# Optimization experiments

Hardware: AMD Instinct MI355X
Metric: run time of the kernel (lower is better)

The kernel has to match this reference:

```python
import jax, jax.numpy as jnp
import numpy as np

B, T, C, H = 8, 2048, 1024, 128

def setup_inputs() -> dict:
    key = jax.random.key(0)
    kx, kq, kk, kv = jax.random.split(key, 4)
    x = jax.random.normal(kx, (B, T, C), dtype=jnp.float32)
    Wq = jax.random.normal(kq, (C, H), dtype=jnp.float32) * 0.02
    Wk = jax.random.normal(kk, (C, H), dtype=jnp.float32) * 0.02
    Wv = jax.random.normal(kv, (C, H), dtype=jnp.float32) * 0.02
    return {"x": x, "Wq": Wq, "Wk": Wk, "Wv": Wv}

def reference(x, Wq, Wk, Wv):
    # q,k,v: [B,T,H] via bias-free dense projections
    q = jnp.einsum('btc,ch->bth', x, Wq)
    k = jnp.einsum('btc,ch->bth', x, Wk)
    v = jnp.einsum('btc,ch->bth', x, Wv)
    scale = k.shape[-1] ** (-0.5)
    # scores: [B,T,T]
    wei = jnp.einsum('bth,bsh->bts', q, k) * scale
    Tlen = x.shape[1]
    causal = jnp.tril(jnp.ones((Tlen, Tlen), dtype=bool))  # True = keep
    wei = jnp.where(causal[None, :, :], wei, -jnp.inf)
    wei = jax.nn.softmax(wei, axis=-1)
    return jnp.einsum('bts,bsh->bth', wei, v)
```

## Files before the change

### kernel.cpp

```cpp
#include <hip/hip_runtime.h>

#define B_ 8
#define T_ 2048
#define C_ 1024
#define H_ 128
#define BT_ (B_*T_)

typedef unsigned short u16;
typedef unsigned int u32;
typedef __attribute__((ext_vector_type(4))) float f32x4;
typedef __attribute__((ext_vector_type(8))) __bf16 bf16x8;

__device__ __forceinline__ u16 f2bf(float f) {
  u32 u = __float_as_uint(f);
  u += 0x7fffu + ((u >> 16) & 1u);
  return (u16)(u >> 16);
}

#define GLL16(g, l) __builtin_amdgcn_global_load_lds( \
    (const __attribute__((address_space(1))) void*)(g), \
    (__attribute__((address_space(3))) void*)(l), 16, 0, 0)

__device__ __forceinline__ bf16x8 load_frag(const u16* base, int stride, int row0, int k0, int lane) {
  const u16* p = base + (size_t)(row0 + (lane & 15)) * stride + k0 + ((lane >> 4) << 3);
  return *reinterpret_cast<const bf16x8*>(p);
}

__device__ __forceinline__ bf16x8 cvt8n(f32x4 lo, f32x4 hi) {
  bf16x8 r;
#pragma unroll
  for (int i = 0; i < 4; i++) { r[i] = (__bf16)lo[i]; r[4 + i] = (__bf16)hi[i]; }
  return r;
}

__global__ void wt_kernel(const float* __restrict__ Wq, const float* __restrict__ Wk,
                          const float* __restrict__ Wv, u16* __restrict__ wt) {
  int mat = blockIdx.y;
  const float* W = (mat == 0) ? Wq : (mat == 1) ? Wk : Wv;
  int i = blockIdx.x * 256 + threadIdx.x;
  int h = i >> 10;
  int c = i & 1023;
  wt[mat * (C_ * H_) + i] = f2bf(W[c * H_ + h]);
}

__global__ __launch_bounds__(512, 4) void qkv_gemm(const float* __restrict__ x, const u16* __restrict__ wt,
                                                   u16* __restrict__ q, u16* __restrict__ k2,
                                                   u16* __restrict__ vt) {
  __shared__ __align__(16) float As[2][64 * 64];
  __shared__ __align__(16) u16 Bs[2][192 * 64];
  int t = threadIdx.x;
  int lane = t & 63, w = t >> 6;
  int wm = w >> 2, wn = w & 3;
  int quad = lane >> 4, col = lane & 15;
  int m0 = blockIdx.x * 64;
  int nb = blockIdx.y * 192;

  int arow = t >> 4;
  int acg = (t & 15) ^ (arow & 15);
  const float* ax0 = x + (size_t)(m0 + arow) * C_ + acg * 4;
  const float* ax1 = ax0 + (size_t)32 * C_;
  int brow = t >> 3;
  int bcg = (t & 7) ^ (brow & 7);
  const u16* bw0 = wt + (size_t)(nb + brow) * C_ + bcg * 8;
  const u16* bw1 = bw0 + (size_t)64 * C_;
  const u16* bw2 = bw0 + (size_t)128 * C_;

#define STAGE(st, buf) do { \
    int ko_ = (st) * 64; \
    GLL16(ax0 + ko_, &As[buf][t * 4]); \
    GLL16(ax1 + ko_, &As[buf][2048 + t * 4]); \
    GLL16(bw0 + ko_, &Bs[buf][t * 8]); \
    GLL16(bw1 + ko_, &Bs[buf][4096 + t * 8]); \
    GLL16(bw2 + ko_, &Bs[buf][8192 + t * 8]); \
  } while (0)

  STAGE(0, 0);

  f32x4 acc[2][3] = {};
#pragma unroll 2
  for (int kk = 0; kk < 16; kk++) {
    int cur = kk & 1;
    __syncthreads();
    if (kk + 1 < 16) STAGE(kk + 1, cur ^ 1);
    const float* Ab = &As[cur][0];
    const u16* Bb = &Bs[cur][0];
#pragma unroll
    for (int ks = 0; ks < 2; ks++) {
      bf16x8 af[2], bfr[3];
#pragma unroll
      for (int mt = 0; mt < 2; mt++) {
        int rr = wm * 32 + mt * 16 + col;
        int s0 = (ks * 8 + quad * 2) ^ (rr & 15);
        int s1 = s0 ^ 1;
        f32x4 lo = *reinterpret_cast<const f32x4*>(Ab + rr * 64 + s0 * 4);
        f32x4 hi = *reinterpret_cast<const f32x4*>(Ab + rr * 64 + s1 * 4);
        af[mt] = cvt8n(lo, hi);
      }
#pragma unroll
      for (int nt = 0; nt < 3; nt++) {
        int rr = wn * 48 + nt * 16 + col;
        int sl = (ks * 4 + quad) ^ (rr & 7);
        bfr[nt] = *reinterpret_cast<const bf16x8*>(Bb + rr * 64 + sl * 8);
      }
#pragma unroll
      for (int mt = 0; mt < 2; mt++)
#pragma unroll
        for (int nt = 0; nt < 3; nt++)
          acc[mt][nt] = __builtin_amdgcn_mfma_f32_16x16x32_bf16(af[mt], bfr[nt], acc[mt][nt], 0, 0, 0);
    }
  }
#undef STAGE

#pragma unroll
  for (int mt = 0; mt < 2; mt++) {
    int row0 = m0 + wm * 32 + mt * 16 + quad * 4;
#pragma unroll
    for (int nt = 0; nt < 3; nt++) {
      int n = nb + wn * 48 + nt * 16 + col;
      int mat = n >> 7, h = n & 127;
      if (mat == 0) {
#pragma unroll
        for (int r = 0; r < 4; r++) q[(size_t)(row0 + r) * H_ + h] = f2bf(acc[mt][nt][r]);
      } else if (mat == 1) {
#pragma unroll
        for (int r = 0; r < 4; r++) k2[(size_t)(row0 + r) * H_ + h] = f2bf(acc[mt][nt][r]);
      } else {
        int bb = row0 >> 11, tt = row0 & 2047;
        ushort4 pk;
        pk.x = f2bf(acc[mt][nt][0]); pk.y = f2bf(acc[mt][nt][1]);
        pk.z = f2bf(acc[mt][nt][2]); pk.w = f2bf(acc[mt][nt][3]);
        *reinterpret_cast<ushort4*>(&vt[((size_t)bb * H_ + h) * T_ + tt]) = pk;
      }
    }
  }
}

__global__ __launch_bounds__(512, 4) void attn_part(const u16* __restrict__ q, const u16* __restrict__ k,
                                                    const u16* __restrict__ vt,
                                                    float* __restrict__ Op, float* __restrict__ lsum) {
  __shared__ __align__(16) u16 Ks[2][32 * 132];
  __shared__ __align__(16) u16 Vs[2][128 * 36];
  __shared__ __align__(16) u16 P[8][16 * 40];
  int t = threadIdx.x;
  int lane = t & 63, w = t >> 6;
  int quad = lane >> 4, col = lane & 15;
  int bx = blockIdx.x;
  int qt = 15 - (bx >> 5);
  int s = (bx >> 3) & 3;
  int b = bx & 7;
  const float scale = 0.08838834764831845f;

  int it0 = s * (qt + 1);
  int it1 = it0 + (qt + 1);

  int krow = t >> 4, ke = (t & 15) * 8;
  int vrow = t >> 2, ve = (t & 3) * 8;

  int qrow0 = b * T_ + qt * 128 + w * 16;
  bf16x8 qf[4];
#pragma unroll
  for (int ks = 0; ks < 4; ks++) qf[ks] = load_frag(q, H_, qrow0, ks * 32, lane);

  f32x4 o[8] = {};
  float l[4] = {0.f, 0.f, 0.f, 0.f};
  int myqrow = qt * 128 + w * 16 + quad * 4;

  {
    const u16* kb = k + (size_t)(b * T_ + it0 * 32) * H_;
    *reinterpret_cast<uint4*>(&Ks[0][krow * 132 + ke]) = *reinterpret_cast<const uint4*>(kb + (size_t)krow * 128 + ke);
    const u16* vb = vt + (size_t)b * H_ * T_ + it0 * 32;
    *reinterpret_cast<uint4*>(&Vs[0][vrow * 36 + ve]) = *reinterpret_cast<const uint4*>(vb + (size_t)vrow * T_ + ve);
  }

  for (int kt = it0; kt < it1; kt++) {
    int cur = (kt - it0) & 1;
    __syncthreads();
    bool more = (kt + 1 < it1);
    uint4 kc, vc;
    if (more) {
      const u16* kb = k + (size_t)(b * T_ + (kt + 1) * 32) * H_;
      kc = *reinterpret_cast<const uint4*>(kb + (size_t)krow * 128 + ke);
      const u16* vb = vt + (size_t)b * H_ * T_ + (kt + 1) * 32;
      vc = *reinterpret_cast<const uint4*>(vb + (size_t)vrow * T_ + ve);
    }

    f32x4 s0 = {}, s1 = {};
#pragma unroll
    for (int ks = 0; ks < 4; ks++) {
      bf16x8 kb0 = *reinterpret_cast<const bf16x8*>(&Ks[cur][col * 132 + ks * 32 + quad * 8]);
      bf16x8 kb1 = *reinterpret_cast<const bf16x8*>(&Ks[cur][(col + 16) * 132 + ks * 32 + quad * 8]);
      s0 = __builtin_amdgcn_mfma_f32_16x16x32_bf16(qf[ks], kb0, s0, 0, 0, 0);
      s1 = __builtin_amdgcn_mfma_f32_16x16x32_bf16(qf[ks], kb1, s1, 0, 0, 0);
    }

    float pv[8];
    int kcol0 = kt * 32 + col;
#pragma unroll
    for (int r = 0; r < 4; r++) {
      int qr = myqrow + r;
      float a0 = fminf(s0[r] * scale, 30.f);
      float a1 = fminf(s1[r] * scale, 30.f);
      a0 = (kcol0      > qr) ? -1e30f : a0;
      a1 = (kcol0 + 16 > qr) ? -1e30f : a1;
      float p0 = __expf(a0);
      float p1 = __expf(a1);
      pv[r] = p0; pv[4 + r] = p1;
      l[r] += p0 + p1;
    }

    u16* Pb = &P[w][0];
#pragma unroll
    for (int r = 0; r < 4; r++) {
      Pb[(quad * 4 + r) * 40 + col] = f2bf(pv[r]);
      Pb[(quad * 4 + r) * 40 + col + 16] = f2bf(pv[4 + r]);
    }
    asm volatile("" ::: "memory");
    __builtin_amdgcn_s_waitcnt(0xc07f);
    asm volatile("" ::: "memory");
    bf16x8 pf = *reinterpret_cast<const bf16x8*>(&Pb[col * 40 + (quad << 3)]);

#pragma unroll
    for (int ht = 0; ht < 8; ht++) {
      bf16x8 vf = *reinterpret_cast<const bf16x8*>(&Vs[cur][(ht * 16 + col) * 36 + quad * 8]);
      o[ht] = __builtin_amdgcn_mfma_f32_16x16x32_bf16(pf, vf, o[ht], 0, 0, 0);
    }

    if (more) {
      int nxt = cur ^ 1;
      *reinterpret_cast<uint4*>(&Ks[nxt][krow * 132 + ke]) = kc;
      *reinterpret_cast<uint4*>(&Vs[nxt][vrow * 36 + ve]) = vc;
    }
  }

#pragma unroll
  for (int r = 0; r < 4; r++) {
    float v = l[r];
    v += __shfl_xor(v, 1);
    v += __shfl_xor(v, 2);
    v += __shfl_xor(v, 4);
    v += __shfl_xor(v, 8);
    l[r] = v;
  }

  int tile = (s * 8 + b) * 16 + qt;
  float* Orow = Op + (size_t)tile * (128 * 128);
  float* lrow = lsum + (size_t)tile * 128;
  int rowin0 = w * 16 + quad * 4;
  if (col == 0) {
#pragma unroll
    for (int r = 0; r < 4; r++) lrow[rowin0 + r] = l[r];
  }
#pragma unroll
  for (int ht = 0; ht < 8; ht++) {
#pragma unroll
    for (int r = 0; r < 4; r++)
      Orow[(size_t)(rowin0 + r) * 128 + ht * 16 + col] = o[ht][r];
  }
}

__global__ __launch_bounds__(256) void attn_comb(const float* __restrict__ Op, const float* __restrict__ lsum,
                                                 float* __restrict__ out) {
  int bx = blockIdx.x;
  int b = bx >> 4, qt = bx & 15;
  int t = threadIdx.x;
  int h = t & 127, half = t >> 7;
  int tile0 = b * 16 + qt;
#pragma unroll 4
  for (int rr = 0; rr < 64; rr++) {
    int row = half * 64 + rr;
    float ls = 0.f, v = 0.f;
#pragma unroll
    for (int p = 0; p < 4; p++) {
      int tp = tile0 + p * 128;
      ls += lsum[tp * 128 + row];
      v  += Op[(size_t)tp * 16384 + row * 128 + h];
    }
    out[((size_t)(b * T_ + qt * 128 + row)) * H_ + h] = v / ls;
  }
}

extern "C" void kernel_launch(void* const* d_in, const int* in_sizes, int n_in,
                              void* d_out, int out_size, void* d_ws, size_t ws_size,
                              hipStream_t stream) {
  (void)in_sizes; (void)n_in; (void)out_size; (void)ws_size;
  const float* x  = (const float*)d_in[0];
  const float* Wq = (const float*)d_in[1];
  const float* Wk = (const float*)d_in[2];
  const float* Wv = (const float*)d_in[3];
  u16* ws = (u16*)d_ws;
  u16* q  = ws;
  u16* k  = ws + (size_t)BT_ * H_;
  u16* vt = ws + 2 * (size_t)BT_ * H_;
  u16* wt = ws + 3 * (size_t)BT_ * H_;
  float* Op = (float*)(ws + 3 * (size_t)BT_ * H_ + 3 * C_ * H_);
  float* lsum = Op + (size_t)512 * 128 * 128;
  float* out = (float*)d_out;

  wt_kernel<<<dim3(512, 3), 256, 0, stream>>>(Wq, Wk, Wv, wt);
  qkv_gemm<<<dim3(BT_ / 64, 2), 512, 0, stream>>>(x, wt, q, k, vt);
  attn_part<<<dim3(512), 512, 0, stream>>>(q, k, vt, Op, lsum);
  attn_comb<<<dim3(128), 256, 0, stream>>>(Op, lsum, out);
}
```

Measured before the change: 157.9 us.

## Give each attention wave two query sub-tiles to reuse K/V fragments

The attention kernel now runs 256 threads (4 waves) per block, and each wave handles 32 query rows as two 16-row halves instead of 16. Each K and V fragment read from shared memory now feeds two MFMAs, which halves LDS reads per MFMA and doubles the K/V tile loads per thread. LDS padding changes (row strides 136 and 40), and P is stored as packed bf16 pairs in 32-bit words, with a shuffle/unpack step rebuilding the MFMA operand. This raises register use (two sets of accumulators and Q fragments) and gives fewer waves per block, which may reduce occupancy and latency hiding.

Result: no change. 160.0 us (+1.3%).

```diff
diff --git a/kernel.cpp b/kernel.cpp
--- a/kernel.cpp
+++ b/kernel.cpp
@@ -135,12 +135,12 @@
   }
 }
 
-__global__ __launch_bounds__(512, 4) void attn_part(const u16* __restrict__ q, const u16* __restrict__ k,
+__global__ __launch_bounds__(256, 2) void attn_part(const u16* __restrict__ q, const u16* __restrict__ k,
                                                     const u16* __restrict__ vt,
                                                     float* __restrict__ Op, float* __restrict__ lsum) {
-  __shared__ __align__(16) u16 Ks[2][32 * 132];
-  __shared__ __align__(16) u16 Vs[2][128 * 36];
-  __shared__ __align__(16) u16 P[8][16 * 40];
+  __shared__ __align__(16) u16 Ks[2][32 * 136];
+  __shared__ __align__(16) u16 Vs[2][128 * 40];
+  __shared__ __align__(16) u32 P32[4][2][16 * 20];
   int t = threadIdx.x;
   int lane = t & 63, w = t >> 6;
   int quad = lane >> 4, col = lane & 15;
@@ -153,108 +153,139 @@
   int it0 = s * (qt + 1);
   int it1 = it0 + (qt + 1);
 
-  int krow = t >> 4, ke = (t & 15) * 8;
-  int vrow = t >> 2, ve = (t & 3) * 8;
-
-  int qrow0 = b * T_ + qt * 128 + w * 16;
-  bf16x8 qf[4];
-#pragma unroll
-  for (int ks = 0; ks < 4; ks++) qf[ks] = load_frag(q, H_, qrow0, ks * 32, lane);
-
-  f32x4 o[8] = {};
-  float l[4] = {0.f, 0.f, 0.f, 0.f};
-  int myqrow = qt * 128 + w * 16 + quad * 4;
+  int krow0 = t >> 4, ke = (t & 15) * 8;
+  int krow1 = krow0 + 16;
+  int vrow0 = t >> 2, ve = (t & 3) * 8;
+  int vrow1 = vrow0 + 64;
+
+  int qrow0 = b * T_ + qt * 128 + w * 32;
+  bf16x8 qf[2][4];
+#pragma unroll
+  for (int hf = 0; hf < 2; hf++)
+#pragma unroll
+    for (int ks = 0; ks < 4; ks++)
+      qf[hf][ks] = load_frag(q, H_, qrow0 + hf * 16, ks * 32, lane);
+
+  f32x4 o[2][8] = {};
+  float l[8] = {};
+  int myqrow = qt * 128 + w * 32 + quad * 4;
 
   {
     const u16* kb = k + (size_t)(b * T_ + it0 * 32) * H_;
-    *reinterpret_cast<uint4*>(&Ks[0][krow * 132 + ke]) = *reinterpret_cast<const uint4*>(kb + (size_t)krow * 128 + ke);
+    *reinterpret_cast<uint4*>(&Ks[0][krow0 * 136 + ke]) = *reinterpret_cast<const uint4*>(kb + (size_t)krow0 * 128 + ke);
+    *reinterpret_cast<uint4*>(&Ks[0][krow1 * 136 + ke]) = *reinterpret_cast<const uint4*>(kb + (size_t)krow1 * 128 + ke);
     const u16* vb = vt + (size_t)b * H_ * T_ + it0 * 32;
-    *reinterpret_cast<uint4*>(&Vs[0][vrow * 36 + ve]) = *reinterpret_cast<const uint4*>(vb + (size_t)vrow * T_ + ve);
+    *reinterpret_cast<uint4*>(&Vs[0][vrow0 * 40 + ve]) = *reinterpret_cast<const uint4*>(vb + (size_t)vrow0 * T_ + ve);
+    *reinterpret_cast<uint4*>(&Vs[0][vrow1 * 40 + ve]) = *reinterpret_cast<const uint4*>(vb + (size_t)vrow1 * T_ + ve);
   }
 
   for (int kt = it0; kt < it1; kt++) {
     int cur = (kt - it0) & 1;
     __syncthreads();
     bool more = (kt + 1 < it1);
-    uint4 kc, vc;
+    uint4 kc0, kc1, vc0, vc1;
     if (more) {
       const u16* kb = k + (size_t)(b * T_ + (kt + 1) * 32) * H_;
-      kc = *reinterpret_cast<const uint4*>(kb + (size_t)krow * 128 + ke);
+      kc0 = *reinterpret_cast<const uint4*>(kb + (size_t)krow0 * 128 + ke);
+      kc1 = *reinterpret_cast<const uint4*>(kb + (size_t)krow1 * 128 + ke);
       const u16* vb = vt + (size_t)b * H_ * T_ + (kt + 1) * 32;
-      vc = *reinterpret_cast<const uint4*>(vb + (size_t)vrow * T_ + ve);
-    }
-
-    f32x4 s0 = {}, s1 = {};
+      vc0 = *reinterpret_cast<const uint4*>(vb + (size_t)vrow0 * T_ + ve);
+      vc1 = *reinterpret_cast<const uint4*>(vb + (size_t)vrow1 * T_ + ve);
+    }
+
+    f32x4 s0[2] = {}, s1[2] = {};
 #pragma unroll
     for (int ks = 0; ks < 4; ks++) {
-      bf16x8 kb0 = *reinterpret_cast<const bf16x8*>(&Ks[cur][col * 132 + ks * 32 + quad * 8]);
-      bf16x8 kb1 = *reinterpret_cast<const bf16x8*>(&Ks[cur][(col + 16) * 132 + ks * 32 + quad * 8]);
-      s0 = __builtin_amdgcn_mfma_f32_16x16x32_bf16(qf[ks], kb0, s0, 0, 0, 0);
-      s1 = __builtin_amdgcn_mfma_f32_16x16x32_bf16(qf[ks], kb1, s1, 0, 0, 0);
-    }
-
-    float pv[8];
+      bf16x8 kb0 = *reinterpret_cast<const bf16x8*>(&Ks[cur][col * 136 + ks * 32 + quad * 8]);
+      bf16x8 kb1 = *reinterpret_cast<const bf16x8*>(&Ks[cur][(col + 16) * 136 + ks * 32 + quad * 8]);
+#pragma unroll
+      for (int hf = 0; hf < 2; hf++) {
+        s0[hf] = __builtin_amdgcn_mfma_f32_16x16x32_bf16(qf[hf][ks], kb0, s0[hf], 0, 0, 0);
+        s1[hf] = __builtin_amdgcn_mfma_f32_16x16x32_bf16(qf[hf][ks], kb1, s1[hf], 0, 0, 0);
+      }
+    }
+
     int kcol0 = kt * 32 + col;
 #pragma unroll
-    for (int r = 0; r < 4; r++) {
-      int qr = myqrow + r;
-      float a0 = fminf(s0[r] * scale, 30.f);
-      float a1 = fminf(s1[r] * scale, 30.f);
-      a0 = (kcol0      > qr) ? -1e30f : a0;
-      a1 = (kcol0 + 16 > qr) ? -1e30f : a1;
-      float p0 = __expf(a0);
-      float p1 = __expf(a1);
-      pv[r] = p0; pv[4 + r] = p1;
-      l[r] += p0 + p1;
-    }
-
-    u16* Pb = &P[w][0];
-#pragma unroll
-    for (int r = 0; r < 4; r++) {
-      Pb[(quad * 4 + r) * 40 + col] = f2bf(pv[r]);
-      Pb[(quad * 4 + r) * 40 + col + 16] = f2bf(pv[4 + r]);
+    for (int hf = 0; hf < 2; hf++) {
+      u32* Pb = &P32[w][hf][0];
+#pragma unroll
+      for (int r = 0; r < 4; r++) {
+        int qr = myqrow + hf * 16 + r;
+        float a0 = fminf(s0[hf][r] * scale, 30.f);
+        float a1 = fminf(s1[hf][r] * scale, 30.f);
+        a0 = (kcol0      > qr) ? -1e30f : a0;
+        a1 = (kcol0 + 16 > qr) ? -1e30f : a1;
+        float p0 = __expf(a0);
+        float p1 = __expf(a1);
+        l[hf * 4 + r] += p0 + p1;
+        Pb[(quad * 4 + r) * 20 + col] = (u32)f2bf(p0) | ((u32)f2bf(p1) << 16);
+      }
     }
     asm volatile("" ::: "memory");
     __builtin_amdgcn_s_waitcnt(0xc07f);
     asm volatile("" ::: "memory");
-    bf16x8 pf = *reinterpret_cast<const bf16x8*>(&Pb[col * 40 + (quad << 3)]);
+
+    bf16x8 pf[2];
+    int j0 = (quad & 1) * 8;
+#pragma unroll
+    for (int hf = 0; hf < 2; hf++) {
+      const u32* Pb = &P32[w][hf][0];
+      uint4 wa = *reinterpret_cast<const uint4*>(&Pb[col * 20 + j0]);
+      uint4 wb = *reinterpret_cast<const uint4*>(&Pb[col * 20 + j0 + 4]);
+      u32 sarr[8] = {wa.x, wa.y, wa.z, wa.w, wb.x, wb.y, wb.z, wb.w};
+      union { u32 u[4]; bf16x8 v; } pu;
+#pragma unroll
+      for (int i = 0; i < 4; i++) {
+        u32 a = sarr[2 * i], c = sarr[2 * i + 1];
+        pu.u[i] = (quad < 2) ? ((a & 0xffffu) | (c << 16))
+                             : ((a >> 16) | (c & 0xffff0000u));
+      }
+      pf[hf] = pu.v;
+    }
 
 #pragma unroll
     for (int ht = 0; ht < 8; ht++) {
-      bf16x8 vf = *reinterpret_cast<const bf16x8*>(&Vs[cur][(ht * 16 + col) * 36 + quad * 8]);
-      o[ht] = __builtin_amdgcn_mfma_f32_16x16x32_bf16(pf, vf, o[ht], 0, 0, 0);
+      bf16x8 vf = *reinterpret_cast<const bf16x8*>(&Vs[cur][(ht * 16 + col) * 40 + quad * 8]);
+      o[0][ht] = __builtin_amdgcn_mfma_f32_16x16x32_bf16(pf[0], vf, o[0][ht], 0, 0, 0);
+      o[1][ht] = __builtin_amdgcn_mfma_f32_16x16x32_bf16(pf[1], vf, o[1][ht], 0, 0, 0);
     }
 
     if (more) {
       int nxt = cur ^ 1;
-      *reinterpret_cast<uint4*>(&Ks[nxt][krow * 132 + ke]) = kc;
-      *reinterpret_cast<uint4*>(&Vs[nxt][vrow * 36 + ve]) = vc;
-    }
-  }
-
-#pragma unroll
-  for (int r = 0; r < 4; r++) {
-    float v = l[r];
+      *reinterpret_cast<uint4*>(&Ks[nxt][krow0 * 136 + ke]) = kc0;
+      *reinterpret_cast<uint4*>(&Ks[nxt][krow1 * 136 + ke]) = kc1;
+      *reinterpret_cast<uint4*>(&Vs[nxt][vrow0 * 40 + ve]) = vc0;
+      *reinterpret_cast<uint4*>(&Vs[nxt][vrow1 * 40 + ve]) = vc1;
+    }
+  }
+
+#pragma unroll
+  for (int i = 0; i < 8; i++) {
+    float v = l[i];
     v += __shfl_xor(v, 1);
     v += __shfl_xor(v, 2);
     v += __shfl_xor(v, 4);
     v += __shfl_xor(v, 8);
-    l[r] = v;
+    l[i] = v;
   }
 
   int tile = (s * 8 + b) * 16 + qt;
   float* Orow = Op + (size_t)tile * (128 * 128);
   float* lrow = lsum + (size_t)tile * 128;
-  int rowin0 = w * 16 + quad * 4;
-  if (col == 0) {
-#pragma unroll
-    for (int r = 0; r < 4; r++) lrow[rowin0 + r] = l[r];
-  }
-#pragma unroll
-  for (int ht = 0; ht < 8; ht++) {
-#pragma unroll
-    for (int r = 0; r < 4; r++)
-      Orow[(size_t)(rowin0 + r) * 128 + ht * 16 + col] = o[ht][r];
+#pragma unroll
+  for (int hf = 0; hf < 2; hf++) {
+    int rowin0 = w * 32 + hf * 16 + quad * 4;
+    if (col == 0) {
+#pragma unroll
+      for (int r = 0; r < 4; r++) lrow[rowin0 + r] = l[hf * 4 + r];
+    }
+#pragma unroll
+    for (int ht = 0; ht < 8; ht++) {
+#pragma unroll
+      for (int r = 0; r < 4; r++)
+        Orow[(size_t)(rowin0 + r) * 128 + ht * 16 + col] = o[hf][ht][r];
+    }
   }
 }
 
@@ -298,6 +329,6 @@
 
   wt_kernel<<<dim3(512, 3), 256, 0, stream>>>(Wq, Wk, Wv, wt);
   qkv_gemm<<<dim3(BT_ / 64, 2), 512, 0, stream>>>(x, wt, q, k, vt);
-  attn_part<<<dim3(512), 512, 0, stream>>>(q, k, vt, Op, lsum);
+  attn_part<<<dim3(512), 256, 0, stream>>>(q, k, vt, Op, lsum);
   attn_comb<<<dim3(128), 256, 0, stream>>>(Op, lsum, out);
 }
```
